# Optimization experiments

Measured on AMD Instinct MI355X. Metric: run time of the kernel, lower is better.

The kernel has to match this reference:

```python
import jax, jax.numpy as jnp
import numpy as np

N = 100000   # nodes
F = 32       # input features
E = 1600000  # edges
G = 512      # graphs
EPS = 1e-5   # BatchNorm eps


def setup_inputs() -> dict:
    key = jax.random.key(0)
    ks = jax.random.split(key, 12)
    x = jax.random.normal(ks[0], (N, F), jnp.float32)
    edge_index = jax.random.randint(ks[1], (2, E), 0, N)
    batch = jnp.sort(jax.random.randint(ks[2], (N,), 0, G))

    def glorot(k, i, o):
        return jax.random.normal(k, (i, o), jnp.float32) * (1.0 / np.sqrt(i))

    return {
        "x": x, "edge_index": edge_index, "batch": batch,
        "W1": glorot(ks[3], F, 16), "b1": jnp.zeros((16,), jnp.float32),
        "g1": jnp.ones((16,), jnp.float32), "be1": jnp.zeros((16,), jnp.float32),
        "W2": glorot(ks[4], 16, 64), "b2": jnp.zeros((64,), jnp.float32),
        "g2": jnp.ones((64,), jnp.float32), "be2": jnp.zeros((64,), jnp.float32),
        "W3": glorot(ks[5], 64, 64), "b3": jnp.zeros((64,), jnp.float32),
        "Wc": glorot(ks[6], 64, 1), "bc": jnp.zeros((1,), jnp.float32),
    }


def _gcn_conv(h, src, dst, dis, W, b, n):
    # PyG GCNConv: D^{-1/2}(A+I)D^{-1/2} X W + b (self-loops folded in analytically)
    hw = h @ W                                   # [N, out]
    msg = hw[src] * (dis[src] * dis[dst])[:, None]   # gather + normalize, [E, out]
    agg = jax.ops.segment_sum(msg, dst, num_segments=n)  # scatter-add
    agg = agg + hw * (dis * dis)[:, None]        # self-loop contribution
    return agg + b


def _bn(h, g, b):
    # BatchNorm1d, training mode (biased variance over node axis)
    m = jnp.mean(h, axis=0)
    v = jnp.mean((h - m) ** 2, axis=0)
    return (h - m) * jax.lax.rsqrt(v + EPS) * g + b


def reference(x, edge_index, batch, W1, b1, g1, be1, W2, b2, g2, be2, W3, b3, Wc, bc):
    n = x.shape[0]
    src, dst = edge_index[0], edge_index[1]
    # degree including self-loops (computed on target nodes, edge weight 1)
    deg = jax.ops.segment_sum(jnp.ones((src.shape[0],), x.dtype), dst, num_segments=n) + 1.0
    dis = jax.lax.rsqrt(deg)

    h = jnp.tanh(_gcn_conv(x, src, dst, dis, W1, b1, n))
    h = _bn(h, g1, be1)
    h = jnp.tanh(_gcn_conv(h, src, dst, dis, W2, b2, n))
    h = _bn(h, g2, be2)
    h = jnp.tanh(_gcn_conv(h, src, dst, dis, W3, b3, n))

    # global_mean_pool over graph ids
    sums = jax.ops.segment_sum(h, batch, num_segments=G)          # [G, 64]
    cnts = jax.ops.segment_sum(jnp.ones((n,), x.dtype), batch, num_segments=G)
    pooled = sums / jnp.maximum(cnts, 1.0)[:, None]

    return pooled @ Wc + bc   # [G, 1]
```

## Files before the change

kernel.cpp:

```cpp
#include <hip/hip_runtime.h>

#define EPSV 1e-5f
#define EB 512
#define NPB 256
#define NBUK_MAX 512

typedef __attribute__((ext_vector_type(8))) short bf16x8;
typedef __attribute__((ext_vector_type(4))) float f32x4;
typedef unsigned short ushort_t;

__device__ inline unsigned f2bf(float f){
  unsigned u = __float_as_uint(f);
  u += 0x7fffu + ((u>>16)&1u);
  return u>>16;
}
#define BF_LO(u) __uint_as_float((u)<<16)
#define BF_HI(u) __uint_as_float((u)&0xffff0000u)
__device__ inline float bfu(unsigned short u){ return __uint_as_float(((unsigned)u)<<16); }

__global__ __launch_bounds__(256) void k_csr_count(const int* __restrict__ dst, int E, int chunk,
                                                   int nbuk, int* __restrict__ cnt){
  __shared__ int hist[NBUK_MAX];
  int t = threadIdx.x, b = blockIdx.x;
  for(int k=t; k<nbuk; k+=256) hist[k]=0;
  __syncthreads();
  int lo = b*chunk, hi = lo+chunk < E ? lo+chunk : E;
  for(int i=lo+t; i<hi; i+=256) atomicAdd(&hist[dst[i]>>8], 1);
  __syncthreads();
  for(int k=t; k<nbuk; k+=256) cnt[(size_t)k*EB + b] = hist[k];
}

__global__ __launch_bounds__(1024) void k_scan_local(const int* __restrict__ v_in, int L,
                                                     int* __restrict__ loc, int* __restrict__ blk){
  __shared__ int ps[1024];
  int t = threadIdx.x;
  int i = blockIdx.x*1024 + t;
  int v = (i < L) ? v_in[i] : 0;
  ps[t] = v;
  __syncthreads();
  for(int off=1; off<1024; off<<=1){
    int u = (t>=off) ? ps[t-off] : 0;
    __syncthreads();
    ps[t] += u;
    __syncthreads();
  }
  if(i < L) loc[i] = ps[t] - v;
  if(t == 1023) blk[blockIdx.x] = ps[t];
}

__global__ __launch_bounds__(1024) void k_scan_sums(int* __restrict__ blk, int nb,
                                                    int* __restrict__ totalOut){
  __shared__ int ps[1024];
  int t = threadIdx.x;
  int v = (t < nb) ? blk[t] : 0;
  ps[t] = v;
  __syncthreads();
  for(int off=1; off<1024; off<<=1){
    int u = (t>=off) ? ps[t-off] : 0;
    __syncthreads();
    ps[t] += u;
    __syncthreads();
  }
  if(t < nb) blk[t] = ps[t] - v;
  if(t == 1023) *totalOut = ps[t];
}

__global__ __launch_bounds__(256) void k_csr_scatter(const int* __restrict__ src,
                                                     const int* __restrict__ dst,
                                                     const int* __restrict__ loc,
                                                     const int* __restrict__ blk,
                                                     int E, int chunk, int nbuk,
                                                     unsigned* __restrict__ epk){
  __shared__ int cur[NBUK_MAX];
  int t = threadIdx.x, b = blockIdx.x;
  for(int k=t; k<nbuk; k+=256){
    int i = k*EB + b;
    cur[k] = loc[i] + blk[i>>10];
  }
  __syncthreads();
  int lo = b*chunk, hi = lo+chunk < E ? lo+chunk : E;
  for(int i=lo+t; i<hi; i+=256){
    int d = dst[i];
    int p = atomicAdd(&cur[d>>8], 1);
    epk[p] = ((unsigned)src[i]<<8) | (unsigned)(d & 255);
  }
}

__global__ __launch_bounds__(256) void k_csr_final(const unsigned* __restrict__ epk,
                                                   const int* __restrict__ loc,
                                                   const int* __restrict__ blk,
                                                   int nbuk, int N, int E,
                                                   int* __restrict__ rp, float* __restrict__ dis,
                                                   int* __restrict__ csr_src){
  __shared__ int hist[NPB], ps[NPB], cur[NPB];
  int t = threadIdx.x, k = blockIdx.x;
  int i0 = k*EB;
  int base = loc[i0] + blk[i0>>10];
  int next;
  if(k+1 < nbuk){ int i1 = (k+1)*EB; next = loc[i1] + blk[i1>>10]; }
  else next = E;
  int cntk = next - base;
  int node0 = k*NPB;
  hist[t] = 0;
  __syncthreads();
  for(int i=t; i<cntk; i+=256) atomicAdd(&hist[(int)(epk[base+i] & 255u)], 1);
  __syncthreads();
  int deg = hist[t];
  ps[t] = deg;
  __syncthreads();
  for(int off=1; off<256; off<<=1){
    int u = (t>=off) ? ps[t-off] : 0;
    __syncthreads();
    ps[t] += u;
    __syncthreads();
  }
  int lb = ps[t] - deg;
  int n = node0 + t;
  if(n < N){
    rp[n]  = base + lb;
    dis[n] = rsqrtf((float)deg + 1.0f);
  }
  cur[t] = base + lb;
  __syncthreads();
  for(int i=t; i<cntk; i+=256){
    unsigned e = epk[base+i];
    int p = atomicAdd(&cur[(int)(e & 255u)], 1);
    csr_src[p] = (int)(e >> 8);
  }
}

__global__ __launch_bounds__(256) void k_gemm1(const float* __restrict__ x,
                                               const float* __restrict__ W,
                                               const float* __restrict__ dis,
                                               int N, ushort_t* __restrict__ Pu){
  __shared__ __align__(16) float Ws[32*16];
  int t = threadIdx.x;
  for(int i=t; i<32*16; i+=256) Ws[i] = W[i];
  __syncthreads();
  int row = blockIdx.x*256 + t;
  if(row >= N) return;
  const float4* xr = (const float4*)(x + (size_t)row*32);
  float acc[16];
  #pragma unroll
  for(int j=0;j<16;j++) acc[j]=0.f;
  #pragma unroll
  for(int k4=0;k4<8;k4++){
    float4 v = xr[k4];
    float vv[4] = {v.x, v.y, v.z, v.w};
    #pragma unroll
    for(int kk=0;kk<4;kk++){
      float h = vv[kk];
      const float* wr = &Ws[(k4*4+kk)*16];
      #pragma unroll
      for(int j=0;j<16;j++) acc[j] += h*wr[j];
    }
  }
  float d = dis[row];
  unsigned q[8];
  #pragma unroll
  for(int j=0;j<8;j++)
    q[j] = f2bf(acc[2*j]*d) | (f2bf(acc[2*j+1]*d)<<16);
  uint4* o = (uint4*)(Pu + (size_t)row*16);
  o[0] = make_uint4(q[0],q[1],q[2],q[3]);
  o[1] = make_uint4(q[4],q[5],q[6],q[7]);
}

template<int C, int CINP, int CIN>
__global__ __launch_bounds__(256) void k_bn_finprep(const float* __restrict__ red,
                           const float* __restrict__ gw, const float* __restrict__ be,
                           float invN, const float* __restrict__ W,
                           ushort_t* __restrict__ wf, float* __restrict__ cp){
  constexpr int HALVES = CINP/32;
  __shared__ float sum0[C], sum1[C], scf[C], shf[C];
  int t = threadIdx.x;
  if(t < 2*C){
    float s = 0.f;
    for(int r=0;r<64;r++) s += red[r*2*C + t];
    if(t < C) sum0[t] = s; else sum1[t-C] = s;
  }
  __syncthreads();
  if(t < C){
    float m = sum0[t]*invN;
    float var = fmaxf(sum1[t]*invN - m*m, 0.f);
    float inv = rsqrtf(var + EPSV);
    float s = gw[t]*inv;
    scf[t] = s;
    shf[t] = be[t] - m*s;
  }
  __syncthreads();
  int total = 4*HALVES*64*8;
  for(int idx=t; idx<total; idx+=256){
    int e = idx & 7;
    int l = (idx>>3) & 63;
    int slot = idx>>9;
    int ct = slot/HALVES, half = slot%HALVES;
    int k = (l>>4)*8 + e + half*32;
    int col = ct*16 + (l&15);
    float v = (k < CIN) ? scf[k]*W[k*64 + col] : 0.f;
    wf[idx] = (ushort_t)f2bf(v);
  }
  if(t < 64){
    float s = 0.f;
    for(int k=0;k<CIN;k++) s += shf[k]*W[k*64 + t];
    cp[t] = s;
  }
}

template<int CINP, int CINA>
__global__ __launch_bounds__(256) void k_gemm_mfma(const ushort_t* __restrict__ Au,
                                                   const ushort_t* __restrict__ wf,
                                                   const float* __restrict__ cp,
                                                   const float* __restrict__ dis,
                                                   int N, ushort_t* __restrict__ Pu){
  constexpr int HALVES = CINP/32;
  int t = threadIdx.x, wid = t>>6, l = t&63;
  int r0 = blockIdx.x*128 + wid*32;

  bf16x8 bfr[4][HALVES];
  #pragma unroll
  for(int ct=0; ct<4; ct++)
    #pragma unroll
    for(int h=0; h<HALVES; h++)
      bfr[ct][h] = *(const bf16x8*)(wf + ((size_t)(ct*HALVES+h)*64 + l)*8);

  bf16x8 af[2][HALVES];
  #pragma unroll
  for(int rt=0; rt<2; rt++){
    int arow = r0 + rt*16 + (l&15);
    int k0 = (l>>4)*8;
    #pragma unroll
    for(int h=0; h<HALVES; h++){
      int kk = k0 + h*32;
      if(arow < N && kk < CINA) af[rt][h] = *(const bf16x8*)(Au + (size_t)arow*CINA + kk);
      else                      af[rt][h] = (bf16x8){0,0,0,0,0,0,0,0};
    }
  }

  f32x4 acc[2][4];
  #pragma unroll
  for(int rt=0; rt<2; rt++)
    #pragma unroll
    for(int ct=0; ct<4; ct++)
      acc[rt][ct] = (f32x4){0.f,0.f,0.f,0.f};

  #pragma unroll
  for(int rt=0; rt<2; rt++)
    #pragma unroll
    for(int ct=0; ct<4; ct++)
      #pragma unroll
      for(int h=0; h<HALVES; h++)
        acc[rt][ct] = __builtin_amdgcn_mfma_f32_16x16x32_bf16(af[rt][h], bfr[ct][h], acc[rt][ct], 0, 0, 0);

  #pragma unroll
  for(int rt=0; rt<2; rt++){
    int rbase = r0 + rt*16 + (l>>4)*4;
    #pragma unroll
    for(int reg=0; reg<4; reg++){
      int row = rbase + reg;
      if(row < N){
        float d = dis[row];
        #pragma unroll
        for(int ct=0; ct<4; ct++){
          int col = ct*16 + (l&15);
          Pu[(size_t)row*64 + col] = (ushort_t)f2bf((acc[rt][ct][reg] + cp[col])*d);
        }
      }
    }
  }
}

template<int C, bool STATS>
__global__ __launch_bounds__(256) void k_gather(const int* __restrict__ rp,
    const int* __restrict__ csr_src,
    const float* __restrict__ dis, const ushort_t* __restrict__ Pu,
    const float* __restrict__ bias, int N, ushort_t* __restrict__ Au,
    float* __restrict__ partials){
  constexpr int GP = C/8;
  int t = threadIdx.x;
  int idx = blockIdx.x*256 + t;
  int n = idx / GP, g = idx % GP;
  bool valid = (n < N);
  float v[8];
  #pragma unroll
  for(int j=0;j<8;j++) v[j]=0.f;

  if(valid){
    int beg = rp[n], end = rp[n+1];
    const uint4* Pv = (const uint4*)Pu;
    uint4 u = Pv[(size_t)n*GP + g];
    float a0 = BF_LO(u.x), a1 = BF_HI(u.x), a2 = BF_LO(u.y), a3 = BF_HI(u.y);
    float a4 = BF_LO(u.z), a5 = BF_HI(u.z), a6 = BF_LO(u.w), a7 = BF_HI(u.w);
    float b0=0.f,b1=0.f,b2=0.f,b3=0.f,b4=0.f,b5=0.f,b6=0.f,b7=0.f;
    int j = beg;
    for(; j+1 < end; j += 2){
      int s0 = csr_src[j], s1 = csr_src[j+1];
      uint4 u0 = Pv[(size_t)s0*GP + g];
      uint4 u1 = Pv[(size_t)s1*GP + g];
      a0 += BF_LO(u0.x); a1 += BF_HI(u0.x); a2 += BF_LO(u0.y); a3 += BF_HI(u0.y);
      a4 += BF_LO(u0.z); a5 += BF_HI(u0.z); a6 += BF_LO(u0.w); a7 += BF_HI(u0.w);
      b0 += BF_LO(u1.x); b1 += BF_HI(u1.x); b2 += BF_LO(u1.y); b3 += BF_HI(u1.y);
      b4 += BF_LO(u1.z); b5 += BF_HI(u1.z); b6 += BF_LO(u1.w); b7 += BF_HI(u1.w);
    }
    if(j < end){
      int s0 = csr_src[j];
      uint4 u0 = Pv[(size_t)s0*GP + g];
      a0 += BF_LO(u0.x); a1 += BF_HI(u0.x); a2 += BF_LO(u0.y); a3 += BF_HI(u0.y);
      a4 += BF_LO(u0.z); a5 += BF_HI(u0.z); a6 += BF_LO(u0.w); a7 += BF_HI(u0.w);
    }
    float d = dis[n];
    float4 bb0 = *(const float4*)(bias + g*8);
    float4 bb1 = *(const float4*)(bias + g*8 + 4);
    v[0] = tanhf((a0+b0)*d + bb0.x); v[1] = tanhf((a1+b1)*d + bb0.y);
    v[2] = tanhf((a2+b2)*d + bb0.z); v[3] = tanhf((a3+b3)*d + bb0.w);
    v[4] = tanhf((a4+b4)*d + bb1.x); v[5] = tanhf((a5+b5)*d + bb1.y);
    v[6] = tanhf((a6+b6)*d + bb1.z); v[7] = tanhf((a7+b7)*d + bb1.w);

    uint4 o;
    o.x = f2bf(v[0]) | (f2bf(v[1])<<16);
    o.y = f2bf(v[2]) | (f2bf(v[3])<<16);
    o.z = f2bf(v[4]) | (f2bf(v[5])<<16);
    o.w = f2bf(v[6]) | (f2bf(v[7])<<16);
    *(uint4*)(Au + (size_t)n*C + g*8) = o;
  }

  if(STATS){
    int lane = t & 63, wid = t >> 6;
    __shared__ float redS[4][GP][8], redQ[4][GP][8];
    #pragma unroll
    for(int j=0;j<8;j++){
      float s = v[j], q = v[j]*v[j];
      #pragma unroll
      for(int off=32; off>=GP; off>>=1){
        s += __shfl_down(s, off, 64);
        q += __shfl_down(q, off, 64);
      }
      if(lane < GP){ redS[wid][lane][j] = s; redQ[wid][lane][j] = q; }
    }
    __syncthreads();
    if(t < C){
      int gg = t>>3, j = t&7;
      float S = redS[0][gg][j]+redS[1][gg][j]+redS[2][gg][j]+redS[3][gg][j];
      float Q = redQ[0][gg][j]+redQ[1][gg][j]+redQ[2][gg][j]+redQ[3][gg][j];
      partials[(size_t)blockIdx.x*2*C + t]     = S;
      partials[(size_t)blockIdx.x*2*C + C + t] = Q;
    }
  }
}

template<int C>
__global__ __launch_bounds__(256) void k_bn_red(const float* __restrict__ partials, int nblk,
                                                float* __restrict__ red){
  constexpr int W = 2*C;
  constexpr int RPF = 256/W;
  int t = threadIdx.x;
  int c = t % W, r0 = t / W;
  float acc = 0.f;
  for(int r = blockIdx.x*RPF + r0; r < nblk; r += 64*RPF)
    acc += partials[(size_t)r*W + c];
  __shared__ float ls[256];
  ls[t] = acc;
  __syncthreads();
  if(t < W){
    float s = 0.f;
    #pragma unroll
    for(int k=0;k<RPF;k++) s += ls[k*W + t];
    red[blockIdx.x*W + t] = s;
  }
}

__global__ __launch_bounds__(256) void k_pool(const ushort_t* __restrict__ Au,
                                              const int* __restrict__ batch, int N,
                                              const float* __restrict__ Wc,
                                              const float* __restrict__ bc,
                                              float* __restrict__ out){
  int gId = blockIdx.x;
  int t = threadIdx.x;
  int lo=0, hi=N;
  while(lo<hi){ int mid=(lo+hi)>>1; if(batch[mid] < gId) lo=mid+1; else hi=mid; }
  int start = lo;
  lo=start; hi=N;
  while(lo<hi){ int mid=(lo+hi)>>1; if(batch[mid] < gId+1) lo=mid+1; else hi=mid; }
  int end = lo;

  int c = t & 63, rg = t >> 6;
  float s = 0.f;
  for(int r = start+rg; r < end; r += 4) s += bfu(Au[(size_t)r*64 + c]);
  __shared__ float ls[256];
  ls[t] = s;
  __syncthreads();
  if(t < 64){
    float tot = ls[t] + ls[64+t] + ls[128+t] + ls[192+t];
    float cnt = (float)(end - start);
    float mean = tot / fmaxf(cnt, 1.0f);
    float v = mean * Wc[t];
    #pragma unroll
    for(int o=32; o>0; o>>=1) v += __shfl_down(v, o, 64);
    if(t == 0) out[gId] = v + bc[0];
  }
}

extern "C" void kernel_launch(void* const* d_in, const int* in_sizes, int n_in,
                              void* d_out, int out_size, void* d_ws, size_t ws_size,
                              hipStream_t stream) {
  const float* x     = (const float*)d_in[0];
  const int*   ei    = (const int*)d_in[1];
  const int*   batch = (const int*)d_in[2];
  const float* W1 = (const float*)d_in[3];
  const float* b1 = (const float*)d_in[4];
  const float* g1 = (const float*)d_in[5];
  const float* be1= (const float*)d_in[6];
  const float* W2 = (const float*)d_in[7];
  const float* b2 = (const float*)d_in[8];
  const float* g2 = (const float*)d_in[9];
  const float* be2= (const float*)d_in[10];
  const float* W3 = (const float*)d_in[11];
  const float* b3 = (const float*)d_in[12];
  const float* Wc = (const float*)d_in[13];
  const float* bc = (const float*)d_in[14];

  int N = in_sizes[2];
  int E = in_sizes[1] / 2;
  int G = out_size;
  const int* srcp = ei;
  const int* dstp = ei + E;
  float* out = (float*)d_out;

  auto cdiv = [](long long a, long long b){ return (int)((a+b-1)/b); };
  int nbuk  = cdiv(N, NPB);
  int chunk = cdiv(E, EB);
  int L     = nbuk * EB;
  int nbL   = cdiv(L, 1024);
  int nblk16 = cdiv((long long)N*2, 256);
  int nblk64 = cdiv((long long)N*8, 256);

  char* w = (char*)d_ws;
  ushort_t* Au       = (ushort_t*)w; w += (size_t)N*64*2;
  ushort_t* Pu       = (ushort_t*)w; w += (size_t)N*64*2;
  float*    dis      = (float*)w;    w += (size_t)N*4;
  int*      row_ptr  = (int*)w;      w += (size_t)(N+1)*4;
  int*      csr_src  = (int*)w;      w += (size_t)E*4;
  unsigned* epk      = (unsigned*)w; w += (size_t)E*4;
  int*      cnt      = (int*)w;      w += (size_t)L*4;
  int*      scan_loc = (int*)w;      w += (size_t)L*4;
  int*      scan_blk = (int*)w;      w += 1024*4;
  float*    partials = (float*)w;    w += (size_t)nblk64*128*4;
  float*    red      = (float*)w;    w += 64*128*4;
  ushort_t* wf       = (ushort_t*)w; w += 8*64*8*2;
  float*    cp       = (float*)w;    w += 64*4;

  k_csr_count<<<EB,256,0,stream>>>(dstp, E, chunk, nbuk, cnt);
  k_scan_local<<<nbL,1024,0,stream>>>(cnt, L, scan_loc, scan_blk);
  k_scan_sums<<<1,1024,0,stream>>>(scan_blk, nbL, row_ptr + N);
  k_csr_scatter<<<EB,256,0,stream>>>(srcp, dstp, scan_loc, scan_blk, E, chunk, nbuk, epk);
  k_csr_final<<<nbuk,256,0,stream>>>(epk, scan_loc, scan_blk, nbuk, N, E, row_ptr, dis, csr_src);

  k_gemm1<<<cdiv(N,256),256,0,stream>>>(x, W1, dis, N, Pu);
  k_gather<16,true><<<nblk16,256,0,stream>>>(row_ptr, csr_src, dis, Pu, b1, N, Au, partials);
  k_bn_red<16><<<64,256,0,stream>>>(partials, nblk16, red);
  k_bn_finprep<16,32,16><<<1,256,0,stream>>>(red, g1, be1, 1.0f/N, W2, wf, cp);

  k_gemm_mfma<32,16><<<cdiv(N,128),256,0,stream>>>(Au, wf, cp, dis, N, Pu);
  k_gather<64,true><<<nblk64,256,0,stream>>>(row_ptr, csr_src, dis, Pu, b2, N, Au, partials);
  k_bn_red<64><<<64,256,0,stream>>>(partials, nblk64, red);
  k_bn_finprep<64,64,64><<<1,256,0,stream>>>(red, g2, be2, 1.0f/N, W3, wf, cp);

  k_gemm_mfma<64,64><<<cdiv(N,128),256,0,stream>>>(Au, wf, cp, dis, N, Pu);
  k_gather<64,false><<<nblk64,256,0,stream>>>(row_ptr, csr_src, dis, Pu, b3, N, Au, partials);

  k_pool<<<G,256,0,stream>>>(Au, batch, N, Wc, bc, out);
}
```

Measured before the change: 217.7 us.

## Aggregate before transform in layers 2-3 and fuse GEMM into gather kernels

Layers 2 and 3 now aggregate the narrower input features first (A·X then W), folding the BatchNorm shift in through a precomputed per-node sum of source dis values. The weight transform then runs inside the gather kernel with FP32 FMA from LDS, replacing the separate MFMA GEMM kernels. This removes two kernel launches and the round trip of the 64-wide P buffer. For layer 2 the gather reads only 16-wide rows instead of 64-wide ones. In exchange, each node does extra scalar FMA work, with edges split across 4 lanes plus shuffle reductions, and bf16 rounding now happens at a different point.

```diff
diff --git a/kernel.cpp b/kernel.cpp
--- a/kernel.cpp
+++ b/kernel.cpp
@@ -5,8 +5,6 @@
 #define NPB 256
 #define NBUK_MAX 512
 
-typedef __attribute__((ext_vector_type(8))) short bf16x8;
-typedef __attribute__((ext_vector_type(4))) float f32x4;
 typedef unsigned short ushort_t;
 
 __device__ inline unsigned f2bf(float f){
@@ -127,12 +125,13 @@
     int p = atomicAdd(&cur[(int)(e & 255u)], 1);
     csr_src[p] = (int)(e >> 8);
   }
+  if(k == nbuk-1 && t == 0) rp[N] = E;
 }
 
 __global__ __launch_bounds__(256) void k_gemm1(const float* __restrict__ x,
                                                const float* __restrict__ W,
                                                const float* __restrict__ dis,
-                                               int N, ushort_t* __restrict__ Pu){
+                                               int N, ushort_t* __restrict__ P1){
   __shared__ __align__(16) float Ws[32*16];
   int t = threadIdx.x;
   for(int i=t; i<32*16; i+=256) Ws[i] = W[i];
@@ -160,142 +159,36 @@
   #pragma unroll
   for(int j=0;j<8;j++)
     q[j] = f2bf(acc[2*j]*d) | (f2bf(acc[2*j+1]*d)<<16);
-  uint4* o = (uint4*)(Pu + (size_t)row*16);
+  uint4* o = (uint4*)(P1 + (size_t)row*16);
   o[0] = make_uint4(q[0],q[1],q[2],q[3]);
   o[1] = make_uint4(q[4],q[5],q[6],q[7]);
 }
 
-template<int C, int CINP, int CIN>
-__global__ __launch_bounds__(256) void k_bn_finprep(const float* __restrict__ red,
-                           const float* __restrict__ gw, const float* __restrict__ be,
-                           float invN, const float* __restrict__ W,
-                           ushort_t* __restrict__ wf, float* __restrict__ cp){
-  constexpr int HALVES = CINP/32;
-  __shared__ float sum0[C], sum1[C], scf[C], shf[C];
-  int t = threadIdx.x;
-  if(t < 2*C){
-    float s = 0.f;
-    for(int r=0;r<64;r++) s += red[r*2*C + t];
-    if(t < C) sum0[t] = s; else sum1[t-C] = s;
-  }
-  __syncthreads();
-  if(t < C){
-    float m = sum0[t]*invN;
-    float var = fmaxf(sum1[t]*invN - m*m, 0.f);
-    float inv = rsqrtf(var + EPSV);
-    float s = gw[t]*inv;
-    scf[t] = s;
-    shf[t] = be[t] - m*s;
-  }
-  __syncthreads();
-  int total = 4*HALVES*64*8;
-  for(int idx=t; idx<total; idx+=256){
-    int e = idx & 7;
-    int l = (idx>>3) & 63;
-    int slot = idx>>9;
-    int ct = slot/HALVES, half = slot%HALVES;
-    int k = (l>>4)*8 + e + half*32;
-    int col = ct*16 + (l&15);
-    float v = (k < CIN) ? scf[k]*W[k*64 + col] : 0.f;
-    wf[idx] = (ushort_t)f2bf(v);
-  }
-  if(t < 64){
-    float s = 0.f;
-    for(int k=0;k<CIN;k++) s += shf[k]*W[k*64 + t];
-    cp[t] = s;
-  }
-}
-
-template<int CINP, int CINA>
-__global__ __launch_bounds__(256) void k_gemm_mfma(const ushort_t* __restrict__ Au,
-                                                   const ushort_t* __restrict__ wf,
-                                                   const float* __restrict__ cp,
-                                                   const float* __restrict__ dis,
-                                                   int N, ushort_t* __restrict__ Pu){
-  constexpr int HALVES = CINP/32;
-  int t = threadIdx.x, wid = t>>6, l = t&63;
-  int r0 = blockIdx.x*128 + wid*32;
-
-  bf16x8 bfr[4][HALVES];
-  #pragma unroll
-  for(int ct=0; ct<4; ct++)
-    #pragma unroll
-    for(int h=0; h<HALVES; h++)
-      bfr[ct][h] = *(const bf16x8*)(wf + ((size_t)(ct*HALVES+h)*64 + l)*8);
-
-  bf16x8 af[2][HALVES];
-  #pragma unroll
-  for(int rt=0; rt<2; rt++){
-    int arow = r0 + rt*16 + (l&15);
-    int k0 = (l>>4)*8;
-    #pragma unroll
-    for(int h=0; h<HALVES; h++){
-      int kk = k0 + h*32;
-      if(arow < N && kk < CINA) af[rt][h] = *(const bf16x8*)(Au + (size_t)arow*CINA + kk);
-      else                      af[rt][h] = (bf16x8){0,0,0,0,0,0,0,0};
-    }
-  }
-
-  f32x4 acc[2][4];
-  #pragma unroll
-  for(int rt=0; rt<2; rt++)
-    #pragma unroll
-    for(int ct=0; ct<4; ct++)
-      acc[rt][ct] = (f32x4){0.f,0.f,0.f,0.f};
-
-  #pragma unroll
-  for(int rt=0; rt<2; rt++)
-    #pragma unroll
-    for(int ct=0; ct<4; ct++)
-      #pragma unroll
-      for(int h=0; h<HALVES; h++)
-        acc[rt][ct] = __builtin_amdgcn_mfma_f32_16x16x32_bf16(af[rt][h], bfr[ct][h], acc[rt][ct], 0, 0, 0);
-
-  #pragma unroll
-  for(int rt=0; rt<2; rt++){
-    int rbase = r0 + rt*16 + (l>>4)*4;
-    #pragma unroll
-    for(int reg=0; reg<4; reg++){
-      int row = rbase + reg;
-      if(row < N){
-        float d = dis[row];
-        #pragma unroll
-        for(int ct=0; ct<4; ct++){
-          int col = ct*16 + (l&15);
-          Pu[(size_t)row*64 + col] = (ushort_t)f2bf((acc[rt][ct][reg] + cp[col])*d);
-        }
-      }
-    }
-  }
-}
-
-template<int C, bool STATS>
-__global__ __launch_bounds__(256) void k_gather(const int* __restrict__ rp,
+__global__ __launch_bounds__(256) void k_gather1(const int* __restrict__ rp,
     const int* __restrict__ csr_src,
-    const float* __restrict__ dis, const ushort_t* __restrict__ Pu,
-    const float* __restrict__ bias, int N, ushort_t* __restrict__ Au,
-    float* __restrict__ partials){
-  constexpr int GP = C/8;
+    const float* __restrict__ dis, const ushort_t* __restrict__ P1,
+    const float* __restrict__ bias, int N, ushort_t* __restrict__ Q1,
+    float* __restrict__ sdis, float* __restrict__ partials){
   int t = threadIdx.x;
   int idx = blockIdx.x*256 + t;
-  int n = idx / GP, g = idx % GP;
-  bool valid = (n < N);
+  int n = idx >> 1, g = t & 1;
   float v[8];
   #pragma unroll
   for(int j=0;j<8;j++) v[j]=0.f;
 
-  if(valid){
+  if(n < N){
     int beg = rp[n], end = rp[n+1];
-    const uint4* Pv = (const uint4*)Pu;
-    uint4 u = Pv[(size_t)n*GP + g];
+    uint4 u = *(const uint4*)(P1 + (size_t)n*16 + g*8);
     float a0 = BF_LO(u.x), a1 = BF_HI(u.x), a2 = BF_LO(u.y), a3 = BF_HI(u.y);
     float a4 = BF_LO(u.z), a5 = BF_HI(u.z), a6 = BF_LO(u.w), a7 = BF_HI(u.w);
     float b0=0.f,b1=0.f,b2=0.f,b3=0.f,b4=0.f,b5=0.f,b6=0.f,b7=0.f;
+    float sd = 0.f;
     int j = beg;
     for(; j+1 < end; j += 2){
       int s0 = csr_src[j], s1 = csr_src[j+1];
-      uint4 u0 = Pv[(size_t)s0*GP + g];
-      uint4 u1 = Pv[(size_t)s1*GP + g];
+      uint4 u0 = *(const uint4*)(P1 + (size_t)s0*16 + g*8);
+      uint4 u1 = *(const uint4*)(P1 + (size_t)s1*16 + g*8);
+      if(g==0) sd += dis[s0] + dis[s1];
       a0 += BF_LO(u0.x); a1 += BF_HI(u0.x); a2 += BF_LO(u0.y); a3 += BF_HI(u0.y);
       a4 += BF_LO(u0.z); a5 += BF_HI(u0.z); a6 += BF_LO(u0.w); a7 += BF_HI(u0.w);
       b0 += BF_LO(u1.x); b1 += BF_HI(u1.x); b2 += BF_LO(u1.y); b3 += BF_HI(u1.y);
@@ -303,7 +196,8 @@
     }
     if(j < end){
       int s0 = csr_src[j];
-      uint4 u0 = Pv[(size_t)s0*GP + g];
+      uint4 u0 = *(const uint4*)(P1 + (size_t)s0*16 + g*8);
+      if(g==0) sd += dis[s0];
       a0 += BF_LO(u0.x); a1 += BF_HI(u0.x); a2 += BF_LO(u0.y); a3 += BF_HI(u0.y);
       a4 += BF_LO(u0.z); a5 += BF_HI(u0.z); a6 += BF_LO(u0.w); a7 += BF_HI(u0.w);
     }
@@ -314,36 +208,34 @@
     v[2] = tanhf((a2+b2)*d + bb0.z); v[3] = tanhf((a3+b3)*d + bb0.w);
     v[4] = tanhf((a4+b4)*d + bb1.x); v[5] = tanhf((a5+b5)*d + bb1.y);
     v[6] = tanhf((a6+b6)*d + bb1.z); v[7] = tanhf((a7+b7)*d + bb1.w);
-
     uint4 o;
-    o.x = f2bf(v[0]) | (f2bf(v[1])<<16);
-    o.y = f2bf(v[2]) | (f2bf(v[3])<<16);
-    o.z = f2bf(v[4]) | (f2bf(v[5])<<16);
-    o.w = f2bf(v[6]) | (f2bf(v[7])<<16);
-    *(uint4*)(Au + (size_t)n*C + g*8) = o;
-  }
-
-  if(STATS){
-    int lane = t & 63, wid = t >> 6;
-    __shared__ float redS[4][GP][8], redQ[4][GP][8];
-    #pragma unroll
-    for(int j=0;j<8;j++){
-      float s = v[j], q = v[j]*v[j];
-      #pragma unroll
-      for(int off=32; off>=GP; off>>=1){
-        s += __shfl_down(s, off, 64);
-        q += __shfl_down(q, off, 64);
-      }
-      if(lane < GP){ redS[wid][lane][j] = s; redQ[wid][lane][j] = q; }
-    }
-    __syncthreads();
-    if(t < C){
-      int gg = t>>3, j = t&7;
-      float S = redS[0][gg][j]+redS[1][gg][j]+redS[2][gg][j]+redS[3][gg][j];
-      float Q = redQ[0][gg][j]+redQ[1][gg][j]+redQ[2][gg][j]+redQ[3][gg][j];
-      partials[(size_t)blockIdx.x*2*C + t]     = S;
-      partials[(size_t)blockIdx.x*2*C + C + t] = Q;
-    }
+    o.x = f2bf(v[0]*d) | (f2bf(v[1]*d)<<16);
+    o.y = f2bf(v[2]*d) | (f2bf(v[3]*d)<<16);
+    o.z = f2bf(v[4]*d) | (f2bf(v[5]*d)<<16);
+    o.w = f2bf(v[6]*d) | (f2bf(v[7]*d)<<16);
+    *(uint4*)(Q1 + (size_t)n*16 + g*8) = o;
+    if(g==0) sdis[n] = sd;
+  }
+
+  int lane = t & 63, wid = t >> 6;
+  __shared__ float redS[4][2][8], redQ[4][2][8];
+  #pragma unroll
+  for(int j=0;j<8;j++){
+    float s = v[j], q = v[j]*v[j];
+    #pragma unroll
+    for(int off=32; off>=2; off>>=1){
+      s += __shfl_down(s, off, 64);
+      q += __shfl_down(q, off, 64);
+    }
+    if(lane < 2){ redS[wid][lane][j] = s; redQ[wid][lane][j] = q; }
+  }
+  __syncthreads();
+  if(t < 16){
+    int gg = t>>3, j = t&7;
+    float S = redS[0][gg][j]+redS[1][gg][j]+redS[2][gg][j]+redS[3][gg][j];
+    float Q = redQ[0][gg][j]+redQ[1][gg][j]+redQ[2][gg][j]+redQ[3][gg][j];
+    partials[(size_t)blockIdx.x*32 + t]      = S;
+    partials[(size_t)blockIdx.x*32 + 16 + t] = Q;
   }
 }
 
@@ -368,7 +260,213 @@
   }
 }
 
-__global__ __launch_bounds__(256) void k_pool(const ushort_t* __restrict__ Au,
+template<int C>
+__global__ __launch_bounds__(256) void k_bn_finprep2(const float* __restrict__ red,
+                           const float* __restrict__ gw, const float* __restrict__ be,
+                           float invN, const float* __restrict__ W,
+                           float* __restrict__ Wp, float* __restrict__ cp){
+  __shared__ float s0[C], s1[C], scf[C], shf[C];
+  int t = threadIdx.x;
+  if(t < 2*C){
+    float s = 0.f;
+    for(int r=0;r<64;r++) s += red[r*2*C + t];
+    if(t < C) s0[t] = s; else s1[t-C] = s;
+  }
+  __syncthreads();
+  if(t < C){
+    float m = s0[t]*invN;
+    float var = fmaxf(s1[t]*invN - m*m, 0.f);
+    float inv = rsqrtf(var + EPSV);
+    float sc = gw[t]*inv;
+    scf[t] = sc;
+    shf[t] = be[t] - m*sc;
+  }
+  __syncthreads();
+  for(int i=t; i<C*64; i+=256){
+    int k = i >> 6;
+    Wp[i] = scf[k]*W[i];
+  }
+  if(t < 64){
+    float s = 0.f;
+    for(int k=0;k<C;k++) s += shf[k]*W[k*64 + t];
+    cp[t] = s;
+  }
+}
+
+__global__ __launch_bounds__(256) void k_l2fused(const int* __restrict__ rp,
+    const int* __restrict__ csr_src, const float* __restrict__ dis,
+    const float* __restrict__ sdis, const ushort_t* __restrict__ Q1,
+    const float* __restrict__ Wp, const float* __restrict__ cp,
+    const float* __restrict__ bias, int N, ushort_t* __restrict__ Q2,
+    float* __restrict__ partials){
+  __shared__ __align__(16) float Wl[16*64];
+  __shared__ float cpl[64], bl[64];
+  int t = threadIdx.x;
+  for(int i=t; i<16*64; i+=256) Wl[i] = Wp[i];
+  if(t < 64){ cpl[t] = cp[t]; bl[t] = bias[t]; }
+  __syncthreads();
+
+  int idx = blockIdx.x*256 + t;
+  int n = idx >> 3, g = t & 7;
+  int half = g & 1, eo = g >> 1;
+  bool valid = (n < N);
+  float M8[8];
+  #pragma unroll
+  for(int j=0;j<8;j++) M8[j]=0.f;
+
+  if(valid){
+    int beg = rp[n], end = rp[n+1];
+    if(eo == 0){
+      uint4 u = *(const uint4*)(Q1 + (size_t)n*16 + half*8);
+      M8[0]+=BF_LO(u.x); M8[1]+=BF_HI(u.x); M8[2]+=BF_LO(u.y); M8[3]+=BF_HI(u.y);
+      M8[4]+=BF_LO(u.z); M8[5]+=BF_HI(u.z); M8[6]+=BF_LO(u.w); M8[7]+=BF_HI(u.w);
+    }
+    for(int j=beg+eo; j<end; j+=4){
+      int s = csr_src[j];
+      uint4 u = *(const uint4*)(Q1 + (size_t)s*16 + half*8);
+      M8[0]+=BF_LO(u.x); M8[1]+=BF_HI(u.x); M8[2]+=BF_LO(u.y); M8[3]+=BF_HI(u.y);
+      M8[4]+=BF_LO(u.z); M8[5]+=BF_HI(u.z); M8[6]+=BF_LO(u.w); M8[7]+=BF_HI(u.w);
+    }
+  }
+  #pragma unroll
+  for(int j=0;j<8;j++){
+    float m = M8[j];
+    m += __shfl_xor(m, 2, 64);
+    m += __shfl_xor(m, 4, 64);
+    M8[j] = m;
+  }
+  float M16[16];
+  #pragma unroll
+  for(int j=0;j<8;j++){
+    float o = __shfl_xor(M8[j], 1, 64);
+    M16[j]   = (half==0) ? M8[j] : o;
+    M16[8+j] = (half==0) ? o     : M8[j];
+  }
+
+  float v[8];
+  #pragma unroll
+  for(int j=0;j<8;j++) v[j]=0.f;
+  if(valid){
+    float d = dis[n];
+    float sg = sdis[n] + d;
+    int c0 = g*8;
+    float acc[8];
+    #pragma unroll
+    for(int j=0;j<8;j++) acc[j] = cpl[c0+j]*sg;
+    #pragma unroll
+    for(int k=0;k<16;k++){
+      float m = M16[k];
+      float4 w0 = *(const float4*)&Wl[k*64 + c0];
+      float4 w1 = *(const float4*)&Wl[k*64 + c0 + 4];
+      acc[0]+=m*w0.x; acc[1]+=m*w0.y; acc[2]+=m*w0.z; acc[3]+=m*w0.w;
+      acc[4]+=m*w1.x; acc[5]+=m*w1.y; acc[6]+=m*w1.z; acc[7]+=m*w1.w;
+    }
+    #pragma unroll
+    for(int j=0;j<8;j++) v[j] = tanhf(d*acc[j] + bl[c0+j]);
+    uint4 o;
+    o.x = f2bf(v[0]*d) | (f2bf(v[1]*d)<<16);
+    o.y = f2bf(v[2]*d) | (f2bf(v[3]*d)<<16);
+    o.z = f2bf(v[4]*d) | (f2bf(v[5]*d)<<16);
+    o.w = f2bf(v[6]*d) | (f2bf(v[7]*d)<<16);
+    *(uint4*)(Q2 + (size_t)n*64 + c0) = o;
+  }
+
+  int lane = t & 63, wid = t >> 6;
+  __shared__ float redS[4][8][8], redQ[4][8][8];
+  #pragma unroll
+  for(int j=0;j<8;j++){
+    float s = v[j], q = v[j]*v[j];
+    #pragma unroll
+    for(int off=32; off>=8; off>>=1){
+      s += __shfl_down(s, off, 64);
+      q += __shfl_down(q, off, 64);
+    }
+    if(lane < 8){ redS[wid][lane][j] = s; redQ[wid][lane][j] = q; }
+  }
+  __syncthreads();
+  if(t < 64){
+    int gg = t>>3, j = t&7;
+    float S = redS[0][gg][j]+redS[1][gg][j]+redS[2][gg][j]+redS[3][gg][j];
+    float Q = redQ[0][gg][j]+redQ[1][gg][j]+redQ[2][gg][j]+redQ[3][gg][j];
+    partials[(size_t)blockIdx.x*128 + t]      = S;
+    partials[(size_t)blockIdx.x*128 + 64 + t] = Q;
+  }
+}
+
+__global__ __launch_bounds__(256) void k_l3fused(const int* __restrict__ rp,
+    const int* __restrict__ csr_src, const float* __restrict__ dis,
+    const float* __restrict__ sdis, const ushort_t* __restrict__ Q2,
+    const float* __restrict__ Wp, const float* __restrict__ cp,
+    const float* __restrict__ bias, int N, ushort_t* __restrict__ H3){
+  __shared__ __align__(16) float Wl[64*64];
+  __shared__ float cpl[64], bl[64];
+  __shared__ float Ml[32][68];
+  int t = threadIdx.x;
+  for(int i=t; i<64*64; i+=256) Wl[i] = Wp[i];
+  if(t < 64){ cpl[t] = cp[t]; bl[t] = bias[t]; }
+  __syncthreads();
+
+  int idx = blockIdx.x*256 + t;
+  int n = idx >> 3, g = t & 7;
+  int nl = t >> 3;
+  bool valid = (n < N);
+  float a0=0.f,a1=0.f,a2=0.f,a3=0.f,a4=0.f,a5=0.f,a6=0.f,a7=0.f;
+  float b0=0.f,b1=0.f,b2=0.f,b3=0.f,b4=0.f,b5=0.f,b6=0.f,b7=0.f;
+
+  if(valid){
+    int beg = rp[n], end = rp[n+1];
+    uint4 u = *(const uint4*)(Q2 + (size_t)n*64 + g*8);
+    a0 += BF_LO(u.x); a1 += BF_HI(u.x); a2 += BF_LO(u.y); a3 += BF_HI(u.y);
+    a4 += BF_LO(u.z); a5 += BF_HI(u.z); a6 += BF_LO(u.w); a7 += BF_HI(u.w);
+    int j = beg;
+    for(; j+1 < end; j += 2){
+      int s0 = csr_src[j], s1 = csr_src[j+1];
+      uint4 u0 = *(const uint4*)(Q2 + (size_t)s0*64 + g*8);
+      uint4 u1 = *(const uint4*)(Q2 + (size_t)s1*64 + g*8);
+      a0 += BF_LO(u0.x); a1 += BF_HI(u0.x); a2 += BF_LO(u0.y); a3 += BF_HI(u0.y);
+      a4 += BF_LO(u0.z); a5 += BF_HI(u0.z); a6 += BF_LO(u0.w); a7 += BF_HI(u0.w);
+      b0 += BF_LO(u1.x); b1 += BF_HI(u1.x); b2 += BF_LO(u1.y); b3 += BF_HI(u1.y);
+      b4 += BF_LO(u1.z); b5 += BF_HI(u1.z); b6 += BF_LO(u1.w); b7 += BF_HI(u1.w);
+    }
+    if(j < end){
+      int s0 = csr_src[j];
+      uint4 u0 = *(const uint4*)(Q2 + (size_t)s0*64 + g*8);
+      a0 += BF_LO(u0.x); a1 += BF_HI(u0.x); a2 += BF_LO(u0.y); a3 += BF_HI(u0.y);
+      a4 += BF_LO(u0.z); a5 += BF_HI(u0.z); a6 += BF_LO(u0.w); a7 += BF_HI(u0.w);
+    }
+  }
+  int c0 = g*8;
+  Ml[nl][c0+0]=a0+b0; Ml[nl][c0+1]=a1+b1; Ml[nl][c0+2]=a2+b2; Ml[nl][c0+3]=a3+b3;
+  Ml[nl][c0+4]=a4+b4; Ml[nl][c0+5]=a5+b5; Ml[nl][c0+6]=a6+b6; Ml[nl][c0+7]=a7+b7;
+  __syncthreads();
+
+  if(valid){
+    float d = dis[n];
+    float sg = sdis[n] + d;
+    float acc[8];
+    #pragma unroll
+    for(int j=0;j<8;j++) acc[j] = cpl[c0+j]*sg;
+    #pragma unroll 8
+    for(int k=0;k<64;k++){
+      float m = Ml[nl][k];
+      float4 w0 = *(const float4*)&Wl[k*64 + c0];
+      float4 w1 = *(const float4*)&Wl[k*64 + c0 + 4];
+      acc[0]+=m*w0.x; acc[1]+=m*w0.y; acc[2]+=m*w0.z; acc[3]+=m*w0.w;
+      acc[4]+=m*w1.x; acc[5]+=m*w1.y; acc[6]+=m*w1.z; acc[7]+=m*w1.w;
+    }
+    float v[8];
+    #pragma unroll
+    for(int j=0;j<8;j++) v[j] = tanhf(d*acc[j] + bl[c0+j]);
+    uint4 o;
+    o.x = f2bf(v[0]) | (f2bf(v[1])<<16);
+    o.y = f2bf(v[2]) | (f2bf(v[3])<<16);
+    o.z = f2bf(v[4]) | (f2bf(v[5])<<16);
+    o.w = f2bf(v[6]) | (f2bf(v[7])<<16);
+    *(uint4*)(H3 + (size_t)n*64 + c0) = o;
+  }
+}
+
+__global__ __launch_bounds__(256) void k_pool(const ushort_t* __restrict__ H3,
                                               const int* __restrict__ batch, int N,
                                               const float* __restrict__ Wc,
                                               const float* __restrict__ bc,
@@ -384,7 +482,7 @@
 
   int c = t & 63, rg = t >> 6;
   float s = 0.f;
-  for(int r = start+rg; r < end; r += 4) s += bfu(Au[(size_t)r*64 + c]);
+  for(int r = start+rg; r < end; r += 4) s += bfu(H3[(size_t)r*64 + c]);
   __shared__ float ls[256];
   ls[t] = s;
   __syncthreads();
@@ -426,6 +524,7 @@
   float* out = (float*)d_out;
 
   auto cdiv = [](long long a, long long b){ return (int)((a+b-1)/b); };
+  auto al16 = [](size_t s){ return (s + 15) & ~(size_t)15; };
   int nbuk  = cdiv(N, NPB);
   int chunk = cdiv(E, EB);
   int L     = nbuk * EB;
@@ -434,19 +533,22 @@
   int nblk64 = cdiv((long long)N*8, 256);
 
   char* w = (char*)d_ws;
-  ushort_t* Au       = (ushort_t*)w; w += (size_t)N*64*2;
-  ushort_t* Pu       = (ushort_t*)w; w += (size_t)N*64*2;
-  float*    dis      = (float*)w;    w += (size_t)N*4;
-  int*      row_ptr  = (int*)w;      w += (size_t)(N+1)*4;
-  int*      csr_src  = (int*)w;      w += (size_t)E*4;
-  unsigned* epk      = (unsigned*)w; w += (size_t)E*4;
-  int*      cnt      = (int*)w;      w += (size_t)L*4;
-  int*      scan_loc = (int*)w;      w += (size_t)L*4;
-  int*      scan_blk = (int*)w;      w += 1024*4;
-  float*    partials = (float*)w;    w += (size_t)nblk64*128*4;
-  float*    red      = (float*)w;    w += 64*128*4;
-  ushort_t* wf       = (ushort_t*)w; w += 8*64*8*2;
-  float*    cp       = (float*)w;    w += 64*4;
+  ushort_t* Q1       = (ushort_t*)w; w += al16((size_t)N*16*2);
+  ushort_t* P1       = (ushort_t*)w; w += al16((size_t)N*16*2);
+  ushort_t* Q2       = (ushort_t*)w; w += al16((size_t)N*64*2);
+  ushort_t* H3       = (ushort_t*)w; w += al16((size_t)N*64*2);
+  float*    dis      = (float*)w;    w += al16((size_t)N*4);
+  float*    sdis     = (float*)w;    w += al16((size_t)N*4);
+  int*      row_ptr  = (int*)w;      w += al16((size_t)(N+1)*4);
+  int*      csr_src  = (int*)w;      w += al16((size_t)E*4);
+  unsigned* epk      = (unsigned*)w; w += al16((size_t)E*4);
+  int*      cnt      = (int*)w;      w += al16((size_t)L*4);
+  int*      scan_loc = (int*)w;      w += al16((size_t)L*4);
+  int*      scan_blk = (int*)w;      w += al16(1024*4);
+  float*    partials = (float*)w;    w += al16((size_t)nblk64*128*4);
+  float*    red      = (float*)w;    w += al16(64*128*4);
+  float*    Wp       = (float*)w;    w += al16(64*64*4);
+  float*    cp       = (float*)w;    w += al16(64*4);
 
   k_csr_count<<<EB,256,0,stream>>>(dstp, E, chunk, nbuk, cnt);
   k_scan_local<<<nbL,1024,0,stream>>>(cnt, L, scan_loc, scan_blk);
@@ -454,18 +556,16 @@
   k_csr_scatter<<<EB,256,0,stream>>>(srcp, dstp, scan_loc, scan_blk, E, chunk, nbuk, epk);
   k_csr_final<<<nbuk,256,0,stream>>>(epk, scan_loc, scan_blk, nbuk, N, E, row_ptr, dis, csr_src);
 
-  k_gemm1<<<cdiv(N,256),256,0,stream>>>(x, W1, dis, N, Pu);
-  k_gather<16,true><<<nblk16,256,0,stream>>>(row_ptr, csr_src, dis, Pu, b1, N, Au, partials);
+  k_gemm1<<<cdiv(N,256),256,0,stream>>>(x, W1, dis, N, P1);
+  k_gather1<<<nblk16,256,0,stream>>>(row_ptr, csr_src, dis, P1, b1, N, Q1, sdis, partials);
   k_bn_red<16><<<64,256,0,stream>>>(partials, nblk16, red);
-  k_bn_finprep<16,32,16><<<1,256,0,stream>>>(red, g1, be1, 1.0f/N, W2, wf, cp);
-
-  k_gemm_mfma<32,16><<<cdiv(N,128),256,0,stream>>>(Au, wf, cp, dis, N, Pu);
-  k_gather<64,true><<<nblk64,256,0,stream>>>(row_ptr, csr_src, dis, Pu, b2, N, Au, partials);
+  k_bn_finprep2<16><<<1,256,0,stream>>>(red, g1, be1, 1.0f/N, W2, Wp, cp);
+
+  k_l2fused<<<nblk64,256,0,stream>>>(row_ptr, csr_src, dis, sdis, Q1, Wp, cp, b2, N, Q2, partials);
   k_bn_red<64><<<64,256,0,stream>>>(partials, nblk64, red);
-  k_bn_finprep<64,64,64><<<1,256,0,stream>>>(red, g2, be2, 1.0f/N, W3, wf, cp);
-
-  k_gemm_mfma<64,64><<<cdiv(N,128),256,0,stream>>>(Au, wf, cp, dis, N, Pu);
-  k_gather<64,false><<<nblk64,256,0,stream>>>(row_ptr, csr_src, dis, Pu, b3, N, Au, partials);
-
-  k_pool<<<G,256,0,stream>>>(Au, batch, N, Wc, bc, out);
-}
+  k_bn_finprep2<64><<<1,256,0,stream>>>(red, g2, be2, 1.0f/N, W3, Wp, cp);
+
+  k_l3fused<<<nblk64,256,0,stream>>>(row_ptr, csr_src, dis, sdis, Q2, Wp, cp, b3, N, H3);
+
+  k_pool<<<G,256,0,stream>>>(H3, batch, N, Wc, bc, out);
+}
```

After: 225.7 us. 1.04x slower.
